# Kernel optimization log

Hardware: AMD Instinct MI355X
Metric: run time of the kernel (lower is better)

Reference implementation:

```python
import jax, jax.numpy as jnp
import numpy as np

DIM = 128
NUM_HEADS = 4
WIN = 16  # effective window: window_size(8) * sqrt(dim_t=4)
N = WIN * WIN
B_ = 512
NW = 64


def _relative_position_index(wh, ww):
    coords = np.stack(np.meshgrid(np.arange(wh), np.arange(ww), indexing='ij'))  # (2,wh,ww)
    cf = coords.reshape(2, -1)
    rel = cf[:, :, None] - cf[:, None, :]  # (2,N,N)
    rel = rel.transpose(1, 2, 0).copy()
    rel[:, :, 0] += wh - 1
    rel[:, :, 1] += ww - 1
    rel[:, :, 0] *= 2 * ww - 1
    return rel.sum(-1).astype(np.int32)  # (N,N)


def setup_inputs() -> dict:
    key = jax.random.key(0)
    ks = jax.random.split(key, 7)
    inputs = jax.random.normal(ks[0], (B_, N, DIM), dtype=jnp.float32)
    mask = jax.random.normal(ks[1], (NW, N, N), dtype=jnp.float32)
    qkv_w = jax.random.normal(ks[2], (3 * DIM, DIM), dtype=jnp.float32) * 0.02
    qkv_b = jnp.zeros((3 * DIM,), dtype=jnp.float32)
    proj_w = jax.random.normal(ks[3], (DIM, DIM), dtype=jnp.float32) * 0.02
    proj_b = jnp.zeros((DIM,), dtype=jnp.float32)
    table_sz = (2 * WIN - 1) * (2 * WIN - 1)  # 961
    bias_table = jax.random.normal(ks[4], (table_sz, NUM_HEADS), dtype=jnp.float32) * 0.02
    rel_idx = jnp.asarray(_relative_position_index(WIN, WIN))  # (N,N) int32
    return {"inputs": inputs, "mask": mask, "qkv_w": qkv_w, "qkv_b": qkv_b,
            "proj_w": proj_w, "proj_b": proj_b, "bias_table": bias_table,
            "rel_idx": rel_idx}


def reference(inputs, mask, qkv_w, qkv_b, proj_w, proj_b, bias_table, rel_idx):
    B, Nn, C = inputs.shape
    H = bias_table.shape[1]
    Dh = C // H
    scale = Dh ** -0.5
    qkv = (inputs @ qkv_w.T + qkv_b).reshape(B, Nn, 3, H, Dh)
    qkv = jnp.transpose(qkv, (2, 0, 3, 1, 4))  # (3,B,H,N,Dh)
    q, k, v = qkv[0] * scale, qkv[1], qkv[2]
    attn = jnp.einsum('bhnd,bhmd->bhnm', q, k)  # (B,H,N,N)
    rpb = jnp.transpose(bias_table[rel_idx], (2, 0, 1))  # (H,N,N)
    attn = attn + rpb[None]
    nW = mask.shape[0]
    attn = attn.reshape(B // nW, nW, H, Nn, Nn) + mask[None, :, None]
    attn = jax.nn.softmax(attn.reshape(B, H, Nn, Nn), axis=-1)
    out = jnp.einsum('bhnm,bhmd->bhnd', attn, v)
    out = jnp.transpose(out, (0, 2, 1, 3)).reshape(B, Nn, C)
    return out @ proj_w.T + proj_b
```

## Files before the change

kernel.cpp:

```cpp
#include <hip/hip_runtime.h>

typedef __bf16 bf16;
typedef __bf16 bf16x8 __attribute__((ext_vector_type(8)));
typedef __bf16 bf16x4 __attribute__((ext_vector_type(4)));
typedef float f32x4 __attribute__((ext_vector_type(4)));

static __device__ __forceinline__ f32x4 mfma16(bf16x8 a, bf16x8 b, f32x4 c) {
  return __builtin_amdgcn_mfma_f32_16x16x32_bf16(a, b, c, 0, 0, 0);
}

static __device__ __forceinline__ bf16x8 ld_bf8(const float* __restrict__ p) {
  f32x4 a = *(const f32x4*)p;
  f32x4 b = *(const f32x4*)(p + 4);
  bf16x8 r;
  r[0] = (bf16)a[0]; r[1] = (bf16)a[1]; r[2] = (bf16)a[2]; r[3] = (bf16)a[3];
  r[4] = (bf16)b[0]; r[5] = (bf16)b[1]; r[6] = (bf16)b[2]; r[7] = (bf16)b[3];
  return r;
}

__global__ void k0_prep(const float* __restrict__ qw, const float* __restrict__ pw,
                        const float* __restrict__ bt, const int* __restrict__ ri,
                        bf16* __restrict__ wb, bf16* __restrict__ pwb,
                        bf16* __restrict__ rb) {
  const int t = blockIdx.x * 256 + threadIdx.x;
  if (blockIdx.x < 64) {
    if (t < 12288) {
      f32x4 v = *(const f32x4*)(qw + (size_t)t * 4);
      bf16x4 o;
#pragma unroll
      for (int r = 0; r < 4; ++r) o[r] = (bf16)v[r];
      *(bf16x4*)(wb + (size_t)t * 4) = o;
    } else {
      const int u = t - 12288;
      f32x4 v = *(const f32x4*)(pw + (size_t)u * 4);
      bf16x4 o;
#pragma unroll
      for (int r = 0; r < 4; ++r) o[r] = (bf16)v[r];
      *(bf16x4*)(pwb + (size_t)u * 4) = o;
    }
  } else {
    const int t2 = t - 16384;
    const int idx = ri[t2];
    f32x4 v = *(const f32x4*)(bt + idx * 4);
#pragma unroll
    for (int h = 0; h < 4; ++h) rb[h * 65536 + t2] = (bf16)v[h];
  }
}

__global__ void __launch_bounds__(512, 2)
k_main(const float* __restrict__ x, const bf16* __restrict__ wb,
       const float* __restrict__ qb, const bf16* __restrict__ pwb,
       const float* __restrict__ pbias, const float* __restrict__ mask,
       const bf16* __restrict__ rb, float* __restrict__ out) {
  __shared__ bf16 ksm[256 * 32];
  __shared__ bf16 vsm[32 * 256];
  __shared__ bf16 psm[8 * 2048];
  const int tid = threadIdx.x, wv = tid >> 6;
  const int ln = tid & 15, qd = (tid >> 4) & 3;
  const int b = blockIdx.x, w = b & 63;
  bf16* pw_ = psm + wv * 2048;

  bf16x8 xf[2][4];
#pragma unroll
  for (int nt = 0; nt < 2; ++nt)
#pragma unroll
    for (int ks = 0; ks < 4; ++ks)
      xf[nt][ks] = ld_bf8(x + (size_t)(b * 256 + wv * 32 + nt * 16 + ln) * 128 +
                          ks * 32 + qd * 8);

  f32x4 acc_out[2][8];
#pragma unroll
  for (int si = 0; si < 2; ++si)
#pragma unroll
    for (int ct2 = 0; ct2 < 8; ++ct2) acc_out[si][ct2] = (f32x4){0.f, 0.f, 0.f, 0.f};

  for (int h = 0; h < 4; ++h) {
    {
      f32x4 aq[2][2];
#pragma unroll
      for (int ct = 0; ct < 2; ++ct)
#pragma unroll
        for (int nt = 0; nt < 2; ++nt) aq[ct][nt] = (f32x4){0.f, 0.f, 0.f, 0.f};
#pragma unroll
      for (int ct = 0; ct < 2; ++ct)
#pragma unroll
        for (int ks = 0; ks < 4; ++ks) {
          bf16x8 wf = *(const bf16x8*)(wb + (size_t)(h * 32 + ct * 16 + ln) * 128 +
                                       ks * 32 + qd * 8);
#pragma unroll
          for (int nt = 0; nt < 2; ++nt) aq[ct][nt] = mfma16(wf, xf[nt][ks], aq[ct][nt]);
        }
#pragma unroll
      for (int ct = 0; ct < 2; ++ct) {
        const int c0 = ct * 16 + qd * 4;
        f32x4 b4 = *(const f32x4*)(qb + h * 32 + c0);
#pragma unroll
        for (int nt = 0; nt < 2; ++nt) {
          bf16x4 o;
#pragma unroll
          for (int r = 0; r < 4; ++r)
            o[r] = (bf16)((aq[ct][nt][r] + b4[r]) * 0.17677669529663689f);
          *(bf16x4*)(pw_ + (nt * 16 + ln) * 32 + c0) = o;
        }
      }
    }
    bf16x8 qf0 = *(const bf16x8*)(pw_ + (0 * 16 + ln) * 32 + qd * 8);
    bf16x8 qf1 = *(const bf16x8*)(pw_ + (1 * 16 + ln) * 32 + qd * 8);

    __syncthreads();

    {
      f32x4 ak[2][2];
#pragma unroll
      for (int ct = 0; ct < 2; ++ct)
#pragma unroll
        for (int nt = 0; nt < 2; ++nt) ak[ct][nt] = (f32x4){0.f, 0.f, 0.f, 0.f};
#pragma unroll
      for (int ct = 0; ct < 2; ++ct)
#pragma unroll
        for (int ks = 0; ks < 4; ++ks) {
          bf16x8 wf = *(const bf16x8*)(wb + (size_t)(128 + h * 32 + ct * 16 + ln) * 128 +
                                       ks * 32 + qd * 8);
#pragma unroll
          for (int nt = 0; nt < 2; ++nt) ak[ct][nt] = mfma16(wf, xf[nt][ks], ak[ct][nt]);
        }
#pragma unroll
      for (int ct = 0; ct < 2; ++ct) {
        const int c0 = ct * 16 + qd * 4;
        f32x4 b4 = *(const f32x4*)(qb + 128 + h * 32 + c0);
        const int slot = ct * 2 + (qd >> 1), off = (qd & 1) * 4;
#pragma unroll
        for (int nt = 0; nt < 2; ++nt) {
          const int grow = wv * 32 + nt * 16 + ln;
          bf16x4 o;
#pragma unroll
          for (int r = 0; r < 4; ++r) o[r] = (bf16)(ak[ct][nt][r] + b4[r]);
          *(bf16x4*)(ksm + grow * 32 + ((slot ^ (grow & 3)) * 8) + off) = o;
        }
      }
      f32x4 av[2][2];
#pragma unroll
      for (int nt = 0; nt < 2; ++nt)
#pragma unroll
        for (int ct = 0; ct < 2; ++ct) av[nt][ct] = (f32x4){0.f, 0.f, 0.f, 0.f};
#pragma unroll
      for (int ks = 0; ks < 4; ++ks)
#pragma unroll
        for (int ct = 0; ct < 2; ++ct) {
          bf16x8 wf = *(const bf16x8*)(wb + (size_t)(256 + h * 32 + ct * 16 + ln) * 128 +
                                       ks * 32 + qd * 8);
#pragma unroll
          for (int nt = 0; nt < 2; ++nt) av[nt][ct] = mfma16(xf[nt][ks], wf, av[nt][ct]);
        }
#pragma unroll
      for (int nt = 0; nt < 2; ++nt)
#pragma unroll
        for (int ct = 0; ct < 2; ++ct) {
          const int c = ct * 16 + ln;
          const float bb = qb[256 + h * 32 + c];
          const int n0 = wv * 32 + nt * 16 + qd * 4;
          const int slot = n0 >> 3, off = (qd & 1) * 4;
          bf16x4 o;
#pragma unroll
          for (int r = 0; r < 4; ++r) o[r] = (bf16)(av[nt][ct][r] + bb);
          *(bf16x4*)(vsm + c * 256 + ((slot ^ (c & 7)) * 8) + off) = o;
        }
    }
    __syncthreads();

#pragma unroll
    for (int si = 0; si < 2; ++si) {
      const bf16x8 qf = si ? qf1 : qf0;
      const int n = wv * 32 + si * 16 + ln;
      float sum = 0.f;
      f32x4 accO[2];
      accO[0] = (f32x4){0.f, 0.f, 0.f, 0.f};
      accO[1] = (f32x4){0.f, 0.f, 0.f, 0.f};
#pragma unroll
      for (int hf = 0; hf < 2; ++hf) {
        f32x4 acc[8];
#pragma unroll
        for (int mt = 0; mt < 8; ++mt) acc[mt] = (f32x4){0.f, 0.f, 0.f, 0.f};
#pragma unroll
        for (int mt = 0; mt < 8; ++mt) {
          const int m = hf * 128 + mt * 16 + ln;
          bf16x8 af = *(const bf16x8*)(ksm + m * 32 + ((qd ^ (m & 3)) * 8));
          acc[mt] = mfma16(af, qf, acc[mt]);
        }
#pragma unroll
        for (int mt = 0; mt < 8; ++mt) {
          const int mcol = hf * 128 + mt * 16 + qd * 4;
          f32x4 m4 = *(const f32x4*)(mask + ((size_t)w * 256 + n) * 256 + mcol);
          bf16x4 r4 = *(const bf16x4*)(rb + (size_t)h * 65536 + n * 256 + mcol);
          bf16x4 pv;
#pragma unroll
          for (int r = 0; r < 4; ++r) {
            float p = __expf(acc[mt][r] + m4[r] + (float)r4[r]);
            sum += p;
            pv[r] = (bf16)p;
          }
          *(bf16x4*)(pw_ + ln * 128 + (((mt * 2 + (qd >> 1)) ^ (ln & 7)) * 8) +
                     (qd & 1) * 4) = pv;
        }
#pragma unroll
        for (int ktl = 0; ktl < 4; ++ktl) {
          const int kt = hf * 4 + ktl;
          bf16x8 pf = *(const bf16x8*)(pw_ + ln * 128 + (((ktl * 4 + qd) ^ (ln & 7)) * 8));
#pragma unroll
          for (int ct = 0; ct < 2; ++ct) {
            const int d = ct * 16 + ln;
            bf16x8 vf = *(const bf16x8*)(vsm + d * 256 + (((kt * 4 + qd) ^ (d & 7)) * 8));
            accO[ct] = mfma16(pf, vf, accO[ct]);
          }
        }
      }
      sum += __shfl_xor(sum, 16);
      sum += __shfl_xor(sum, 32);
      const float linv = 1.0f / sum;
#pragma unroll
      for (int r = 0; r < 4; ++r) {
        const float lb = __shfl(linv, qd * 4 + r);
#pragma unroll
        for (int ct = 0; ct < 2; ++ct)
          pw_[(qd * 4 + r) * 40 + ct * 16 + ln] = (bf16)(accO[ct][r] * lb);
      }
      bf16x8 aof = *(const bf16x8*)(pw_ + ln * 40 + qd * 8);
#pragma unroll
      for (int ct2 = 0; ct2 < 8; ++ct2) {
        bf16x8 wpf = *(const bf16x8*)(pwb + (size_t)(ct2 * 16 + ln) * 128 + h * 32 +
                                      qd * 8);
        acc_out[si][ct2] = mfma16(aof, wpf, acc_out[si][ct2]);
      }
    }
  }

#pragma unroll
  for (int si = 0; si < 2; ++si)
#pragma unroll
    for (int ct2 = 0; ct2 < 8; ++ct2) {
      const int col = ct2 * 16 + ln;
      const float bb = pbias[col];
#pragma unroll
      for (int r = 0; r < 4; ++r)
        out[(size_t)(b * 256 + wv * 32 + si * 16 + qd * 4 + r) * 128 + col] =
            acc_out[si][ct2][r] + bb;
    }
}

extern "C" void kernel_launch(void* const* d_in, const int* in_sizes, int n_in,
                              void* d_out, int out_size, void* d_ws, size_t ws_size,
                              hipStream_t stream) {
  const float* x = (const float*)d_in[0];
  const float* mask = (const float*)d_in[1];
  const float* qkv_w = (const float*)d_in[2];
  const float* qkv_b = (const float*)d_in[3];
  const float* proj_w = (const float*)d_in[4];
  const float* proj_b = (const float*)d_in[5];
  const float* bias_table = (const float*)d_in[6];
  const int* rel_idx = (const int*)d_in[7];

  char* ws = (char*)d_ws;
  bf16* wb = (bf16*)ws;
  bf16* pwb = (bf16*)(ws + 98304);
  bf16* rb = (bf16*)(ws + 131072);

  k0_prep<<<dim3(320), dim3(256), 0, stream>>>(qkv_w, proj_w, bias_table, rel_idx,
                                               wb, pwb, rb);
  k_main<<<dim3(512), dim3(512), 0, stream>>>(x, wb, qkv_b, pwb, proj_b, mask, rb,
                                              (float*)d_out);
}
```

Measured before the change: 374.2 us.

## Pre-convert attention mask to bf16 in prep kernel and relax launch bounds

Adds a pass in the prep kernel that converts the fp32 window mask to bf16 in workspace. The main attention kernel then reads half as many mask bytes on each of its repeated per-head, per-batch mask loads. The launch bound minimum blocks per CU drops from 2 to 1, giving the compiler more register room at the cost of potential occupancy. The extra prep pass adds a full read and write of the mask, and rounding the mask to bf16 slightly reduces accuracy.

```diff
diff --git a/kernel.cpp b/kernel.cpp
--- a/kernel.cpp
+++ b/kernel.cpp
@@ -20,10 +20,12 @@
 
 __global__ void k0_prep(const float* __restrict__ qw, const float* __restrict__ pw,
                         const float* __restrict__ bt, const int* __restrict__ ri,
-                        bf16* __restrict__ wb, bf16* __restrict__ pwb,
-                        bf16* __restrict__ rb) {
-  const int t = blockIdx.x * 256 + threadIdx.x;
-  if (blockIdx.x < 64) {
+                        const float* __restrict__ mask, bf16* __restrict__ wb,
+                        bf16* __restrict__ pwb, bf16* __restrict__ rb,
+                        bf16* __restrict__ mb) {
+  const int bid = blockIdx.x;
+  if (bid < 64) {
+    const int t = bid * 256 + threadIdx.x;
     if (t < 12288) {
       f32x4 v = *(const f32x4*)(qw + (size_t)t * 4);
       bf16x4 o;
@@ -38,19 +40,30 @@
       for (int r = 0; r < 4; ++r) o[r] = (bf16)v[r];
       *(bf16x4*)(pwb + (size_t)u * 4) = o;
     }
-  } else {
-    const int t2 = t - 16384;
+  } else if (bid < 320) {
+    const int t2 = (bid - 64) * 256 + threadIdx.x;
     const int idx = ri[t2];
     f32x4 v = *(const f32x4*)(bt + idx * 4);
 #pragma unroll
     for (int h = 0; h < 4; ++h) rb[h * 65536 + t2] = (bf16)v[h];
+  } else {
+    const int mid = bid - 320;
+#pragma unroll
+    for (int it = 0; it < 4; ++it) {
+      const size_t t = (size_t)mid * 1024 + it * 256 + threadIdx.x;
+      f32x4 m4 = *(const f32x4*)(mask + t * 4);
+      bf16x4 o;
+#pragma unroll
+      for (int r = 0; r < 4; ++r) o[r] = (bf16)m4[r];
+      *(bf16x4*)(mb + t * 4) = o;
+    }
   }
 }
 
-__global__ void __launch_bounds__(512, 2)
+__global__ void __launch_bounds__(512, 1)
 k_main(const float* __restrict__ x, const bf16* __restrict__ wb,
        const float* __restrict__ qb, const bf16* __restrict__ pwb,
-       const float* __restrict__ pbias, const float* __restrict__ mask,
+       const float* __restrict__ pbias, const bf16* __restrict__ mb,
        const bf16* __restrict__ rb, float* __restrict__ out) {
   __shared__ bf16 ksm[256 * 32];
   __shared__ bf16 vsm[32 * 256];
@@ -190,12 +203,12 @@
 #pragma unroll
         for (int mt = 0; mt < 8; ++mt) {
           const int mcol = hf * 128 + mt * 16 + qd * 4;
-          f32x4 m4 = *(const f32x4*)(mask + ((size_t)w * 256 + n) * 256 + mcol);
+          bf16x4 m4 = *(const bf16x4*)(mb + ((size_t)w * 256 + n) * 256 + mcol);
           bf16x4 r4 = *(const bf16x4*)(rb + (size_t)h * 65536 + n * 256 + mcol);
           bf16x4 pv;
 #pragma unroll
           for (int r = 0; r < 4; ++r) {
-            float p = __expf(acc[mt][r] + m4[r] + (float)r4[r]);
+            float p = __expf(acc[mt][r] + (float)m4[r] + (float)r4[r]);
             sum += p;
             pv[r] = (bf16)p;
           }
@@ -263,9 +276,10 @@
   bf16* wb = (bf16*)ws;
   bf16* pwb = (bf16*)(ws + 98304);
   bf16* rb = (bf16*)(ws + 131072);
-
-  k0_prep<<<dim3(320), dim3(256), 0, stream>>>(qkv_w, proj_w, bias_table, rel_idx,
-                                               wb, pwb, rb);
-  k_main<<<dim3(512), dim3(512), 0, stream>>>(x, wb, qkv_b, pwb, proj_b, mask, rb,
+  bf16* mb = (bf16*)(ws + 655360);
+
+  k0_prep<<<dim3(1344), dim3(256), 0, stream>>>(qkv_w, proj_w, bias_table, rel_idx,
+                                                mask, wb, pwb, rb, mb);
+  k_main<<<dim3(512), dim3(512), 0, stream>>>(x, wb, qkv_b, pwb, proj_b, mb, rb,
                                               (float*)d_out);
 }
```

New measurement: 478.4 us. +27.9%, slower.
